# Kernel optimization log

Measured on AMD Instinct MI355X. Metric: run time of the kernel, lower is better.

## Reference

```python
import jax, jax.numpy as jnp
import numpy as np

WIN = 64  # win_y == win_x == 64 in the original


def setup_inputs() -> dict:
    key = jax.random.key(0)
    k1, k2 = jax.random.split(key)
    B, C, H, W = 16, 1, 1024, 1024
    pred = jax.random.uniform(k1, (B, C, H, W), dtype=jnp.float32)
    target = jax.random.uniform(k2, (B, C, H, W), dtype=jnp.float32)
    return {"pred": pred, "target": target}


def _iou_loss(patch_pred, patch_target):
    # Vectorized over batch: sum_i (1 - Iand_i / Ior_i)
    iand = jnp.sum(patch_target * patch_pred, axis=(1, 2, 3))  # [B]
    ior = jnp.sum(patch_target, axis=(1, 2, 3)) + jnp.sum(patch_pred, axis=(1, 2, 3)) - iand
    return jnp.sum(1.0 - iand / ior)


def reference(pred, target):
    # Faithful to the source: anchors iterate over target.shape[0] (batch)
    # and target.shape[1] (channels) in steps of 64, but slice SPATIAL dims.
    # With B=16, C=1 this yields a single (0,0) anchor -> the top-left
    # 64x64 spatial patch. Loop bounds are static -> jit-compatible.
    B, C = target.shape[0], target.shape[1]
    iou_loss = jnp.float32(0.0)
    for anchor_y in range(0, B, WIN):
        for anchor_x in range(0, C, WIN):
            pp = pred[:, :, anchor_y:anchor_y + WIN, anchor_x:anchor_x + WIN]
            pt = target[:, :, anchor_y:anchor_y + WIN, anchor_x:anchor_x + WIN]
            iou_loss = iou_loss + _iou_loss(pp, pt)
    return iou_loss
```

## Files before the change

### kernel.cpp

```cpp
#include <hip/hip_runtime.h>


#define B_   16
#define HW_  (1024 * 1024)
#define WROW 1024

__global__ __launch_bounds__(256)
void patch_iou_partial(const float* __restrict__ pred,
                       const float* __restrict__ targ,
                       float* __restrict__ ws) {
    const int j = blockIdx.x;
    const int b = j >> 2;
    const int q = j & 3;
    const int t = threadIdx.x;

    const int row  = (q << 4) + (t >> 4);
    const int col4 = t & 15;
    const size_t base = (size_t)b * HW_ + (size_t)row * WROW + (size_t)(col4 << 2);

    const float4 p  = *(const float4*)(pred + base);
    const float4 tg = *(const float4*)(targ + base);

    float sp  = p.x + p.y + p.z + p.w;
    float st  = tg.x + tg.y + tg.z + tg.w;
    float spt = p.x * tg.x + p.y * tg.y + p.z * tg.z + p.w * tg.w;

    #pragma unroll
    for (int off = 32; off > 0; off >>= 1) {
        sp  += __shfl_down(sp,  off, 64);
        st  += __shfl_down(st,  off, 64);
        spt += __shfl_down(spt, off, 64);
    }

    __shared__ float red[3][4];
    const int wave = t >> 6;
    const int lane = t & 63;
    if (lane == 0) {
        red[0][wave] = sp;
        red[1][wave] = st;
        red[2][wave] = spt;
    }
    __syncthreads();
    if (t == 0) {
        const float a = red[0][0] + red[0][1] + red[0][2] + red[0][3];
        const float c = red[1][0] + red[1][1] + red[1][2] + red[1][3];
        const float d = red[2][0] + red[2][1] + red[2][2] + red[2][3];
        ws[j * 3 + 0] = a;
        ws[j * 3 + 1] = c;
        ws[j * 3 + 2] = d;
    }
}

__global__ __launch_bounds__(64)
void patch_iou_final(const float* __restrict__ ws, float* __restrict__ out) {
    const int lane = threadIdx.x;
    float term = 0.0f;
    if (lane < B_) {
        float sp = 0.0f, st = 0.0f, spt = 0.0f;
        #pragma unroll
        for (int q = 0; q < 4; ++q) {
            const int j = (lane << 2) + q;
            sp  += ws[j * 3 + 0];
            st  += ws[j * 3 + 1];
            spt += ws[j * 3 + 2];
        }
        const float ior = st + sp - spt;
        term = 1.0f - spt / ior;
    }
    #pragma unroll
    for (int off = 8; off > 0; off >>= 1) {
        term += __shfl_down(term, off, 64);
    }
    if (lane == 0) out[0] = term;
}

extern "C" void kernel_launch(void* const* d_in, const int* in_sizes, int n_in,
                              void* d_out, int out_size, void* d_ws, size_t ws_size,
                              hipStream_t stream) {
    const float* pred = (const float*)d_in[0];
    const float* targ = (const float*)d_in[1];
    float* out = (float*)d_out;
    float* ws  = (float*)d_ws;

    patch_iou_partial<<<64, 256, 0, stream>>>(pred, targ, ws);
    patch_iou_final<<<1, 64, 0, stream>>>(ws, out);
}
```

Measured before the change: 116.5 us.

## Fuse partial and final IoU reductions into one cooperative kernel with grid sync

Replaces the two-kernel scheme (64 partial blocks plus a final reduction kernel) with a single cooperative launch of 16 blocks, one per batch item. Each thread now loops over four row groups, and each block writes its per-batch IoU term directly. A grid-wide sync then lets block 0 sum the terms. This removes the second kernel launch and its dependency gap, at the cost of cooperative-launch overhead and grid-sync latency, and it uses fewer blocks for the loads.

```diff
diff --git a/kernel.cpp b/kernel.cpp
--- a/kernel.cpp
+++ b/kernel.cpp
@@ -1,4 +1,7 @@
 #include <hip/hip_runtime.h>
+#include <hip/hip_cooperative_groups.h>
+
+namespace cg = cooperative_groups;
 
 
 #define B_   16
@@ -6,24 +9,26 @@
 #define WROW 1024
 
 __global__ __launch_bounds__(256)
-void patch_iou_partial(const float* __restrict__ pred,
-                       const float* __restrict__ targ,
-                       float* __restrict__ ws) {
-    const int j = blockIdx.x;
-    const int b = j >> 2;
-    const int q = j & 3;
+void patch_iou_fused(const float* __restrict__ pred,
+                     const float* __restrict__ targ,
+                     float* __restrict__ ws,
+                     float* __restrict__ out) {
+    const int b = blockIdx.x;
     const int t = threadIdx.x;
 
-    const int row  = (q << 4) + (t >> 4);
     const int col4 = t & 15;
-    const size_t base = (size_t)b * HW_ + (size_t)row * WROW + (size_t)(col4 << 2);
-
-    const float4 p  = *(const float4*)(pred + base);
-    const float4 tg = *(const float4*)(targ + base);
-
-    float sp  = p.x + p.y + p.z + p.w;
-    float st  = tg.x + tg.y + tg.z + tg.w;
-    float spt = p.x * tg.x + p.y * tg.y + p.z * tg.z + p.w * tg.w;
+    const int rbase = t >> 4;
+    float sp = 0.0f, st = 0.0f, spt = 0.0f;
+    #pragma unroll
+    for (int q = 0; q < 4; ++q) {
+        const int row = (q << 4) + rbase;
+        const size_t base = (size_t)b * HW_ + (size_t)row * WROW + (size_t)(col4 << 2);
+        const float4 p  = *(const float4*)(pred + base);
+        const float4 tg = *(const float4*)(targ + base);
+        sp  += p.x + p.y + p.z + p.w;
+        st  += tg.x + tg.y + tg.z + tg.w;
+        spt += p.x * tg.x + p.y * tg.y + p.z * tg.z + p.w * tg.w;
+    }
 
     #pragma unroll
     for (int off = 32; off > 0; off >>= 1) {
@@ -45,33 +50,17 @@
         const float a = red[0][0] + red[0][1] + red[0][2] + red[0][3];
         const float c = red[1][0] + red[1][1] + red[1][2] + red[1][3];
         const float d = red[2][0] + red[2][1] + red[2][2] + red[2][3];
-        ws[j * 3 + 0] = a;
-        ws[j * 3 + 1] = c;
-        ws[j * 3 + 2] = d;
+        ws[b] = 1.0f - d / (a + c - d);
     }
-}
 
-__global__ __launch_bounds__(64)
-void patch_iou_final(const float* __restrict__ ws, float* __restrict__ out) {
-    const int lane = threadIdx.x;
-    float term = 0.0f;
-    if (lane < B_) {
-        float sp = 0.0f, st = 0.0f, spt = 0.0f;
+    cg::this_grid().sync();
+
+    if (b == 0 && t == 0) {
+        float s = 0.0f;
         #pragma unroll
-        for (int q = 0; q < 4; ++q) {
-            const int j = (lane << 2) + q;
-            sp  += ws[j * 3 + 0];
-            st  += ws[j * 3 + 1];
-            spt += ws[j * 3 + 2];
-        }
-        const float ior = st + sp - spt;
-        term = 1.0f - spt / ior;
+        for (int i = 0; i < B_; ++i) s += ws[i];
+        out[0] = s;
     }
-    #pragma unroll
-    for (int off = 8; off > 0; off >>= 1) {
-        term += __shfl_down(term, off, 64);
-    }
-    if (lane == 0) out[0] = term;
 }
 
 extern "C" void kernel_launch(void* const* d_in, const int* in_sizes, int n_in,
@@ -82,6 +71,7 @@
     float* out = (float*)d_out;
     float* ws  = (float*)d_ws;
 
-    patch_iou_partial<<<64, 256, 0, stream>>>(pred, targ, ws);
-    patch_iou_final<<<1, 64, 0, stream>>>(ws, out);
+    void* args[] = { (void*)&pred, (void*)&targ, (void*)&ws, (void*)&out };
+    hipLaunchCooperativeKernel((const void*)patch_iou_fused,
+                               dim3(B_), dim3(256), args, 0, stream);
 }
```

New measurement: 138.9 us. +19.2%, slower.
